# Kernel optimization log

Hardware: AMD Instinct MI355X
Metric: run time of the kernel (lower is better)

Reference implementation:

```python
import jax, jax.numpy as jnp
import numpy as np
from jax import lax

B, L, V, E, F, C, K = 8, 2500, 50000, 100, 50, 8921, 10
PAD = K // 2  # padding=floor(filter_size/2) -> output length L+1 for even K


def setup_inputs() -> dict:
    key = jax.random.key(0)
    ks = jax.random.split(key, 7)
    text = jax.random.randint(ks[0], (B, L), 0, V, dtype=jnp.int32)
    embed_weight = jax.random.normal(ks[1], (V, E), jnp.float32) * 0.1
    embed_weight = embed_weight.at[0].set(0.0)  # padding_idx=0
    conv_w = jax.random.normal(ks[2], (F, E, K), jnp.float32) * (2.0 / (E * K + F)) ** 0.5
    conv_b = jnp.zeros((F,), jnp.float32)
    Q_w = jax.random.normal(ks[3], (C, F), jnp.float32) * (2.0 / (C + F)) ** 0.5
    out_w = jax.random.normal(ks[4], (C, F), jnp.float32) * (2.0 / (C + F)) ** 0.5
    out_b = jnp.zeros((C,), jnp.float32)
    return {"text": text, "embed_weight": embed_weight, "conv_w": conv_w,
            "conv_b": conv_b, "Q_w": Q_w, "out_w": out_w, "out_b": out_b}


def reference(text, embed_weight, conv_w, conv_b, Q_w, out_w, out_b):
    # Embedding lookup (dropout omitted: eval mode): (B, L, E)
    x = embed_weight[text]
    # Conv1d over length: torch Conv1d(E, F, K, padding=PAD)
    x = jnp.transpose(x, (0, 2, 1))  # (B, E, L)
    z = lax.conv_general_dilated(x, conv_w, window_strides=(1,),
                                 padding=[(PAD, PAD)],
                                 dimension_numbers=("NCH", "OIH", "NCH"))
    z = z + conv_b[None, :, None]
    Z = jnp.tanh(jnp.transpose(z, (0, 2, 1)))  # (B, L', F), L' = L+1
    # Per-label attention: Q_w (C,F) @ Z^T -> (B, C, L'), softmax over length
    scores = jnp.einsum("cf,blf->bcl", Q_w, Z)
    alpha = jax.nn.softmax(scores, axis=2)  # (B, C, L')
    # Attention-weighted sum: (B, C, F)
    Ecf = jnp.einsum("bcl,blf->bcf", alpha, Z)
    # Per-class dot-product readout
    logits = jnp.sum(out_w[None] * Ecf, axis=2) + out_b  # (B, C)
    return logits, alpha
```

## Files before the change

### kernel.cpp

```cpp
#include <hip/hip_runtime.h>
#include <math.h>

#define BB 8
#define LL 2500
#define VV 50000
#define EE 100
#define FF 50
#define CC 8921
#define KK 10
#define PADW 5
#define LOUT 2501
#define NLT 157
#define LPAD (NLT * 16)
#define NCT 140
#define NT16 (NCT * 4)
#define NG 10

typedef __attribute__((ext_vector_type(8))) short bf16x8;
typedef __attribute__((ext_vector_type(4))) float f32x4;

__device__ __forceinline__ short to_bf16(float f) {
  unsigned u = __builtin_bit_cast(unsigned, f);
  u += 0x7FFFu + ((u >> 16) & 1u);
  return (short)(u >> 16);
}

__global__ void k1_conv(const int* __restrict__ text,
                        const float* __restrict__ embed,
                        const float* __restrict__ convw,
                        const float* __restrict__ convb,
                        short* __restrict__ Z16) {
  __shared__ float xw[73 * 101];
  const int b   = blockIdx.y;
  const int l0  = blockIdx.x * 64;
  const int tid = threadIdx.x;

  for (int idx = tid; idx < 73 * 100; idx += 256) {
    int r = idx / 100;
    int e = idx - r * 100;
    int t = l0 - PADW + r;
    float v = 0.f;
    if (t >= 0 && t < LL) {
      int tok = text[b * LL + t];
      v = embed[tok * EE + e];
    }
    xw[r * 101 + e] = v;
  }
  __syncthreads();

  const int ll = tid & 63;
  const int fg = __builtin_amdgcn_readfirstlane(tid >> 6);
  const int l  = l0 + ll;

  float acc[13];
#pragma unroll
  for (int j = 0; j < 13; ++j) {
    int f = fg + 4 * j;
    acc[j] = (f < FF) ? convb[f] : 0.f;
  }

  for (int e = 0; e < EE; ++e) {
    float xk[KK];
#pragma unroll
    for (int k = 0; k < KK; ++k) xk[k] = xw[(ll + k) * 101 + e];
#pragma unroll
    for (int j = 0; j < 13; ++j) {
      int f = fg + 4 * j;
      if (f < FF) {
        const float* wp = convw + (f * EE + e) * KK;
#pragma unroll
        for (int k = 0; k < KK; ++k) acc[j] += xk[k] * wp[k];
      }
    }
  }

  if (l < LPAD) {
#pragma unroll
    for (int j = 0; j < 13; ++j) {
      int f = fg + 4 * j;
      if (f < FF) {
        float v = (l < LOUT) ? tanhf(acc[j]) : 0.f;
        Z16[((size_t)b * LPAD + l) * 64 + f] = to_bf16(v);
      }
    }
  }
  for (int idx = tid; idx < 64 * 14; idx += 256) {
    int r = idx / 14, k = 50 + idx % 14;
    int lz = l0 + r;
    if (lz < LPAD) Z16[((size_t)b * LPAD + lz) * 64 + k] = 0;
  }
}

__global__ void k_packW(const float* __restrict__ W, short* __restrict__ Wp) {
  int u = blockIdx.x * 256 + threadIdx.x;
  int lane = u & 63, kh = (u >> 6) & 1, t16 = u >> 7;
  int c  = t16 * 16 + (lane & 15);
  int k0 = 4 * (lane >> 4) + 32 * kh;
  union { short s[8]; uint4 v; } o;
#pragma unroll
  for (int j = 0; j < 8; ++j) {
    int k = k0 + (j & 3) + 16 * (j >> 2);
    float val = (c < CC && k < FF) ? W[c * FF + k] : 0.f;
    o.s[j] = to_bf16(val);
  }
  ((uint4*)Wp)[u] = o.v;
}

__global__ void k_packZ(const short* __restrict__ Z16, short* __restrict__ Zp) {
  int u = blockIdx.x * 256 + threadIdx.x;
  int lane = u & 63, kh = (u >> 6) & 1, t = u >> 7;
  int lt = t % NLT, b = t / NLT;
  int l  = lt * 16 + (lane & 15);
  int k0 = 4 * (lane >> 4) + 32 * kh;
  const short* src = Z16 + ((size_t)b * LPAD + l) * 64 + k0;
  uint2 a  = *(const uint2*)src;
  uint2 bb = *(const uint2*)(src + 16);
  uint4 o; o.x = a.x; o.y = a.y; o.z = bb.x; o.w = bb.y;
  ((uint4*)Zp)[u] = o;
}

__global__ __launch_bounds__(256) void k_attn(
    const short* __restrict__ Zp, const short* __restrict__ Qp,
    const short* __restrict__ Op, const float* __restrict__ outb,
    float* __restrict__ alpha, float* __restrict__ logits) {
  const int id   = blockIdx.x;
  const int b    = id & 7;
  const int ct   = id >> 3;
  const int tid  = threadIdx.x;
  const int w    = tid >> 6;
  const int lane = tid & 63;
  const int g    = lane >> 4, col = lane & 15;
  const int cb   = ct * 64;

  __shared__ float red[4][4][4][4];
  __shared__ float rdinv[64];
  __shared__ float sA[4 * 16 * 68];

  bf16x8 qf[4][2], of[4][2];
#pragma unroll
  for (int mf = 0; mf < 4; ++mf)
#pragma unroll
    for (int kh = 0; kh < 2; ++kh) {
      int t16 = ct * 4 + mf;
      qf[mf][kh] = ((const bf16x8*)Qp)[(t16 * 2 + kh) * 64 + lane];
      of[mf][kh] = ((const bf16x8*)Op)[(t16 * 2 + kh) * 64 + lane];
    }
  const bf16x8* Zb = (const bf16x8*)Zp + (size_t)b * NLT * 2 * 64;

  float dacc[4][4];
#pragma unroll
  for (int mf = 0; mf < 4; ++mf)
#pragma unroll
    for (int r = 0; r < 4; ++r) dacc[mf][r] = 0.f;

  for (int t = 0; t < NG; ++t) {
    const int lt0 = t * 16 + w * 4;
    bf16x8 zz[4][2];
#pragma unroll
    for (int i = 0; i < 4; ++i) {
      int lt = lt0 + i; if (lt > NLT - 1) lt = NLT - 1;
      zz[i][0] = Zb[(lt * 2 + 0) * 64 + lane];
      zz[i][1] = Zb[(lt * 2 + 1) * 64 + lane];
    }
#pragma unroll
    for (int i = 0; i < 4; ++i) {
      int   l    = (lt0 + i) * 16 + col;
      float lmsk = (l < LOUT) ? 1.f : 0.f;
#pragma unroll
      for (int mf = 0; mf < 4; ++mf) {
        f32x4 acc = {0.f, 0.f, 0.f, 0.f};
        acc = __builtin_amdgcn_mfma_f32_16x16x32_bf16(qf[mf][0], zz[i][0], acc, 0, 0, 0);
        acc = __builtin_amdgcn_mfma_f32_16x16x32_bf16(qf[mf][1], zz[i][1], acc, 0, 0, 0);
#pragma unroll
        for (int r = 0; r < 4; ++r) dacc[mf][r] += lmsk * __expf(acc[r]);
      }
    }
  }

#pragma unroll
  for (int mf = 0; mf < 4; ++mf)
#pragma unroll
    for (int r = 0; r < 4; ++r) {
      float v = dacc[mf][r];
      v += __shfl_xor(v, 1); v += __shfl_xor(v, 2);
      v += __shfl_xor(v, 4); v += __shfl_xor(v, 8);
      dacc[mf][r] = v;
    }
  if (col == 0)
#pragma unroll
    for (int mf = 0; mf < 4; ++mf)
#pragma unroll
      for (int r = 0; r < 4; ++r) red[w][mf][g][r] = dacc[mf][r];
  __syncthreads();
  if (tid < 64) {
    int mf = tid >> 4, gg = (tid >> 2) & 3, r = tid & 3;
    float s = red[0][mf][gg][r] + red[1][mf][gg][r] +
              red[2][mf][gg][r] + red[3][mf][gg][r];
    rdinv[tid] = 1.f / s;
  }
  __syncthreads();

  float rd[4][4];
#pragma unroll
  for (int mf = 0; mf < 4; ++mf)
#pragma unroll
    for (int r = 0; r < 4; ++r) rd[mf][r] = rdinv[mf * 16 + g * 4 + r];

  float lacc[4][4];
#pragma unroll
  for (int mf = 0; mf < 4; ++mf)
#pragma unroll
    for (int r = 0; r < 4; ++r) lacc[mf][r] = 0.f;

  float* sAw = sA + w * (16 * 68);

  for (int t = 0; t < NG; ++t) {
    const int lt0 = t * 16 + w * 4;
    bf16x8 zz[4][2];
#pragma unroll
    for (int i = 0; i < 4; ++i) {
      int lt = lt0 + i; if (lt > NLT - 1) lt = NLT - 1;
      zz[i][0] = Zb[(lt * 2 + 0) * 64 + lane];
      zz[i][1] = Zb[(lt * 2 + 1) * 64 + lane];
    }
#pragma unroll
    for (int mf = 0; mf < 4; ++mf) {
#pragma unroll
      for (int i = 0; i < 4; ++i) {
        f32x4 s = {0.f, 0.f, 0.f, 0.f}, tt = {0.f, 0.f, 0.f, 0.f};
        s  = __builtin_amdgcn_mfma_f32_16x16x32_bf16(qf[mf][0], zz[i][0], s, 0, 0, 0);
        s  = __builtin_amdgcn_mfma_f32_16x16x32_bf16(qf[mf][1], zz[i][1], s, 0, 0, 0);
        tt = __builtin_amdgcn_mfma_f32_16x16x32_bf16(of[mf][0], zz[i][0], tt, 0, 0, 0);
        tt = __builtin_amdgcn_mfma_f32_16x16x32_bf16(of[mf][1], zz[i][1], tt, 0, 0, 0);
        int l = (lt0 + i) * 16 + col;
#pragma unroll
        for (int r = 0; r < 4; ++r) {
          float a = __expf(s[r]) * rd[mf][r];
          lacc[mf][r] += (l < LOUT) ? a * tt[r] : 0.f;
          sAw[(g * 4 + r) * 68 + i * 16 + col] = a;
        }
      }
      const int l0w = lt0 * 16;
      const int lw  = l0w + lane;
#pragma unroll
      for (int rr = 0; rr < 16; ++rr) {
        int c = cb + mf * 16 + rr;
        if (lw < LOUT && c < CC)
          alpha[(size_t)(b * CC + c) * LOUT + lw] = sAw[rr * 68 + lane];
      }
    }
  }

#pragma unroll
  for (int mf = 0; mf < 4; ++mf)
#pragma unroll
    for (int r = 0; r < 4; ++r) {
      float v = lacc[mf][r];
      v += __shfl_xor(v, 1); v += __shfl_xor(v, 2);
      v += __shfl_xor(v, 4); v += __shfl_xor(v, 8);
      lacc[mf][r] = v;
    }
  __syncthreads();
  if (col == 0)
#pragma unroll
    for (int mf = 0; mf < 4; ++mf)
#pragma unroll
      for (int r = 0; r < 4; ++r) red[w][mf][g][r] = lacc[mf][r];
  __syncthreads();
  if (tid < 64) {
    int mf = tid >> 4, gg = (tid >> 2) & 3, r = tid & 3;
    int c = cb + tid;
    if (c < CC) {
      float v = red[0][mf][gg][r] + red[1][mf][gg][r] +
                red[2][mf][gg][r] + red[3][mf][gg][r];
      logits[b * CC + c] = v + outb[c];
    }
  }
}

extern "C" void kernel_launch(void* const* d_in, const int* in_sizes, int n_in,
                              void* d_out, int out_size, void* d_ws, size_t ws_size,
                              hipStream_t stream) {
  const int*   text  = (const int*)d_in[0];
  const float* embed = (const float*)d_in[1];
  const float* convw = (const float*)d_in[2];
  const float* convb = (const float*)d_in[3];
  const float* Qw    = (const float*)d_in[4];
  const float* outw  = (const float*)d_in[5];
  const float* outb  = (const float*)d_in[6];

  float* out    = (float*)d_out;
  float* logits = out;
  float* alpha  = out + (size_t)BB * CC;

  short* Z16 = (short*)alpha;

  short* wsS = (short*)d_ws;
  short* Zp  = wsS;
  short* Qp  = Zp + (size_t)BB * NLT * 2 * 64 * 8;
  short* Op  = Qp + (size_t)NT16 * 2 * 64 * 8;

  k1_conv<<<dim3((LPAD + 63) / 64, BB), 256, 0, stream>>>(
      text, embed, convw, convb, Z16);
  k_packW<<<(NT16 * 128) / 256, 256, 0, stream>>>(Qw, Qp);
  k_packW<<<(NT16 * 128) / 256, 256, 0, stream>>>(outw, Op);
  k_packZ<<<(BB * NLT * 128) / 256, 256, 0, stream>>>(Z16, Zp);
  k_attn<<<dim3(NCT * BB), 256, 0, stream>>>(Zp, Qp, Op, outb, alpha, logits);
}
```

Before: 693.8 us.

## Stream Z tiles with register double-buffering, raise occupancy, use nontemporal alpha stores

```diff
diff --git a/kernel.cpp b/kernel.cpp
--- a/kernel.cpp
+++ b/kernel.cpp
@@ -15,6 +15,7 @@
 #define NCT 140
 #define NT16 (NCT * 4)
 #define NG 10
+#define NU 40
 
 typedef __attribute__((ext_vector_type(8))) short bf16x8;
 typedef __attribute__((ext_vector_type(4))) float f32x4;
@@ -119,7 +120,7 @@
   ((uint4*)Zp)[u] = o;
 }
 
-__global__ __launch_bounds__(256) void k_attn(
+__global__ __launch_bounds__(256, 2) void k_attn(
     const short* __restrict__ Zp, const short* __restrict__ Qp,
     const short* __restrict__ Op, const float* __restrict__ outb,
     float* __restrict__ alpha, float* __restrict__ logits) {
@@ -153,24 +154,27 @@
 #pragma unroll
     for (int r = 0; r < 4; ++r) dacc[mf][r] = 0.f;
 
-  for (int t = 0; t < NG; ++t) {
-    const int lt0 = t * 16 + w * 4;
-    bf16x8 zz[4][2];
-#pragma unroll
-    for (int i = 0; i < 4; ++i) {
-      int lt = lt0 + i; if (lt > NLT - 1) lt = NLT - 1;
-      zz[i][0] = Zb[(lt * 2 + 0) * 64 + lane];
-      zz[i][1] = Zb[(lt * 2 + 1) * 64 + lane];
-    }
-#pragma unroll
-    for (int i = 0; i < 4; ++i) {
-      int   l    = (lt0 + i) * 16 + col;
-      float lmsk = (l < LOUT) ? 1.f : 0.f;
+  {
+    bf16x8 zc0, zc1, zn0, zn1;
+    int lt0c = (w * 4 > NLT - 1) ? NLT - 1 : w * 4;
+    zn0 = Zb[(lt0c * 2 + 0) * 64 + lane];
+    zn1 = Zb[(lt0c * 2 + 1) * 64 + lane];
+    for (int u = 0; u < NU; ++u) {
+      zc0 = zn0; zc1 = zn1;
+      const int lt_cur = (u >> 2) * 16 + w * 4 + (u & 3);
+      if (u + 1 < NU) {
+        int nlt = ((u + 1) >> 2) * 16 + w * 4 + ((u + 1) & 3);
+        if (nlt > NLT - 1) nlt = NLT - 1;
+        zn0 = Zb[(nlt * 2 + 0) * 64 + lane];
+        zn1 = Zb[(nlt * 2 + 1) * 64 + lane];
+      }
+      const int   l    = lt_cur * 16 + col;
+      const float lmsk = (l < LOUT) ? 1.f : 0.f;
 #pragma unroll
       for (int mf = 0; mf < 4; ++mf) {
         f32x4 acc = {0.f, 0.f, 0.f, 0.f};
-        acc = __builtin_amdgcn_mfma_f32_16x16x32_bf16(qf[mf][0], zz[i][0], acc, 0, 0, 0);
-        acc = __builtin_amdgcn_mfma_f32_16x16x32_bf16(qf[mf][1], zz[i][1], acc, 0, 0, 0);
+        acc = __builtin_amdgcn_mfma_f32_16x16x32_bf16(qf[mf][0], zc0, acc, 0, 0, 0);
+        acc = __builtin_amdgcn_mfma_f32_16x16x32_bf16(qf[mf][1], zc1, acc, 0, 0, 0);
 #pragma unroll
         for (int r = 0; r < 4; ++r) dacc[mf][r] += lmsk * __expf(acc[r]);
       }
@@ -214,39 +218,45 @@
 
   float* sAw = sA + w * (16 * 68);
 
-  for (int t = 0; t < NG; ++t) {
-    const int lt0 = t * 16 + w * 4;
-    bf16x8 zz[4][2];
-#pragma unroll
-    for (int i = 0; i < 4; ++i) {
-      int lt = lt0 + i; if (lt > NLT - 1) lt = NLT - 1;
-      zz[i][0] = Zb[(lt * 2 + 0) * 64 + lane];
-      zz[i][1] = Zb[(lt * 2 + 1) * 64 + lane];
-    }
-#pragma unroll
-    for (int mf = 0; mf < 4; ++mf) {
-#pragma unroll
-      for (int i = 0; i < 4; ++i) {
-        f32x4 s = {0.f, 0.f, 0.f, 0.f}, tt = {0.f, 0.f, 0.f, 0.f};
-        s  = __builtin_amdgcn_mfma_f32_16x16x32_bf16(qf[mf][0], zz[i][0], s, 0, 0, 0);
-        s  = __builtin_amdgcn_mfma_f32_16x16x32_bf16(qf[mf][1], zz[i][1], s, 0, 0, 0);
-        tt = __builtin_amdgcn_mfma_f32_16x16x32_bf16(of[mf][0], zz[i][0], tt, 0, 0, 0);
-        tt = __builtin_amdgcn_mfma_f32_16x16x32_bf16(of[mf][1], zz[i][1], tt, 0, 0, 0);
-        int l = (lt0 + i) * 16 + col;
-#pragma unroll
-        for (int r = 0; r < 4; ++r) {
-          float a = __expf(s[r]) * rd[mf][r];
-          lacc[mf][r] += (l < LOUT) ? a * tt[r] : 0.f;
-          sAw[(g * 4 + r) * 68 + i * 16 + col] = a;
+  for (int mf = 0; mf < 4; ++mf) {
+    bf16x8 zc0, zc1, zn0, zn1;
+    int lt0c = (w * 4 > NLT - 1) ? NLT - 1 : w * 4;
+    zn0 = Zb[(lt0c * 2 + 0) * 64 + lane];
+    zn1 = Zb[(lt0c * 2 + 1) * 64 + lane];
+    for (int u = 0; u < NU; ++u) {
+      zc0 = zn0; zc1 = zn1;
+      const int lt_cur = (u >> 2) * 16 + w * 4 + (u & 3);
+      if (u + 1 < NU) {
+        int nlt = ((u + 1) >> 2) * 16 + w * 4 + ((u + 1) & 3);
+        if (nlt > NLT - 1) nlt = NLT - 1;
+        zn0 = Zb[(nlt * 2 + 0) * 64 + lane];
+        zn1 = Zb[(nlt * 2 + 1) * 64 + lane];
+      }
+      f32x4 s = {0.f, 0.f, 0.f, 0.f}, tt = {0.f, 0.f, 0.f, 0.f};
+      s  = __builtin_amdgcn_mfma_f32_16x16x32_bf16(qf[mf][0], zc0, s, 0, 0, 0);
+      s  = __builtin_amdgcn_mfma_f32_16x16x32_bf16(qf[mf][1], zc1, s, 0, 0, 0);
+      tt = __builtin_amdgcn_mfma_f32_16x16x32_bf16(of[mf][0], zc0, tt, 0, 0, 0);
+      tt = __builtin_amdgcn_mfma_f32_16x16x32_bf16(of[mf][1], zc1, tt, 0, 0, 0);
+      const int l = lt_cur * 16 + col;
+#pragma unroll
+      for (int r = 0; r < 4; ++r) {
+        float a = __expf(s[r]) * rd[mf][r];
+        lacc[mf][r] += (l < LOUT) ? a * tt[r] : 0.f;
+        sAw[(g * 4 + r) * 68 + (u & 3) * 16 + col] = a;
+      }
+      if ((u & 3) == 3) {
+        const int l0w = (u >> 2) * 256 + w * 64;
+        const int lw  = l0w + lane;
+        if (lw < LOUT) {
+          const int crow = cb + mf * 16;
+          size_t base = ((size_t)(b * CC + crow)) * LOUT + lw;
+#pragma unroll
+          for (int rr = 0; rr < 16; ++rr) {
+            if (crow + rr < CC)
+              __builtin_nontemporal_store(sAw[rr * 68 + lane],
+                                          &alpha[base + (size_t)rr * LOUT]);
+          }
         }
-      }
-      const int l0w = lt0 * 16;
-      const int lw  = l0w + lane;
-#pragma unroll
-      for (int rr = 0; rr < 16; ++rr) {
-        int c = cb + mf * 16 + rr;
-        if (lw < LOUT && c < CC)
-          alpha[(size_t)(b * CC + c) * LOUT + lw] = sAw[rr * 68 + lane];
       }
     }
   }
```

Measured after the change: 704.4 us. No clear change (+1.5%).
